# Optimization experiments

Hardware: AMD Instinct MI355X
Metric: run time of the kernel (lower is better)

Reference implementation:

```python
import jax, jax.numpy as jnp
import numpy as np

DIM = 512
NUM_HEADS = 8
HEAD_DIM = DIM // NUM_HEADS
SCALE = HEAD_DIM ** -0.5


def setup_inputs() -> dict:
    key = jax.random.key(0)
    ks = jax.random.split(key, 10)
    B, Sq, Skv = 4, 2048, 2048
    std = DIM ** -0.5
    return {
        "x1": jax.random.normal(ks[0], (B, Sq, DIM), jnp.float32),
        "x2": jax.random.normal(ks[1], (B, Skv, DIM), jnp.float32),
        "Wq": jax.random.normal(ks[2], (DIM, DIM), jnp.float32) * std,
        "bq": jax.random.normal(ks[3], (DIM,), jnp.float32) * 0.02,
        "Wk": jax.random.normal(ks[4], (DIM, DIM), jnp.float32) * std,
        "bk": jax.random.normal(ks[5], (DIM,), jnp.float32) * 0.02,
        "Wv": jax.random.normal(ks[6], (DIM, DIM), jnp.float32) * std,
        "bv": jax.random.normal(ks[7], (DIM,), jnp.float32) * 0.02,
        "Wo": jax.random.normal(ks[8], (DIM, DIM), jnp.float32) * std,
        "bo": jax.random.normal(ks[9], (DIM,), jnp.float32) * 0.02,
    }


def reference(x1, x2, Wq, bq, Wk, bk, Wv, bv, Wo, bo):
    B, Sq, _ = x1.shape
    Skv = x2.shape[1]
    # Linear projections (torch nn.Linear: x @ W.T + b)
    Q = (x1 @ Wq.T + bq).reshape(B, Sq, NUM_HEADS, HEAD_DIM)
    K = (x2 @ Wk.T + bk).reshape(B, Skv, NUM_HEADS, HEAD_DIM)
    V = (x2 @ Wv.T + bv).reshape(B, Skv, NUM_HEADS, HEAD_DIM)
    # [B, H, Sq, Skv]
    attn = jnp.einsum("bqhd,bkhd->bhqk", Q, K) * SCALE
    attn = jax.nn.softmax(attn, axis=-1)  # dropout is identity in eval mode
    out = jnp.einsum("bhqk,bkhd->bqhd", attn, V).reshape(B, Sq, DIM)
    return out @ Wo.T + bo
```

## Files before the change

kernel.cpp:

```cpp
#include <hip/hip_runtime.h>
#include <math.h>

constexpr int kB = 4, kS = 2048, kDim = 512, kNH = 8, kHD = 64;
constexpr float kQScale = 0.18033688011112042f;

using bf16x8 = __attribute__((ext_vector_type(8))) short;
using f32x4  = __attribute__((ext_vector_type(4))) float;

__device__ __forceinline__ unsigned pack_rn(float f0, float f1) {
  unsigned a = __builtin_bit_cast(unsigned, f0) + 0x8000u;
  unsigned b = __builtin_bit_cast(unsigned, f1) + 0x8000u;
  return __builtin_amdgcn_perm(b, a, 0x07060302u);
}
__device__ __forceinline__ unsigned short f2bf_rn(float f) {
  return (unsigned short)((__builtin_bit_cast(unsigned, f) + 0x8000u) >> 16);
}
__device__ __forceinline__ float fexp2(float x) {
#if __has_builtin(__builtin_amdgcn_exp2f)
  return __builtin_amdgcn_exp2f(x);
#else
  return exp2f(x);
#endif
}

#define GLDS(gp, lp) __builtin_amdgcn_global_load_lds(                         \
    (const __attribute__((address_space(1))) void*)(gp),                       \
    (__attribute__((address_space(3))) void*)(lp), 16, 0, 0)

__global__ __launch_bounds__(256) void cvt_bf16(
    const float* __restrict__ x1, const float* __restrict__ x2,
    const float* __restrict__ Wq, const float* __restrict__ Wk,
    const float* __restrict__ Wv, const float* __restrict__ Wo,
    unsigned short* __restrict__ x1b, unsigned short* __restrict__ x2b,
    unsigned short* __restrict__ wb) {
  const size_t i = (size_t)blockIdx.x * 256 + threadIdx.x;
  const float* src;
  unsigned short* dst;
  size_t off;
  if (i < 1048576) { src = x1; dst = x1b; off = i; }
  else if (i < 2097152) { src = x2; dst = x2b; off = i - 1048576; }
  else {
    const size_t j = i - 2097152;
    const int seg = (int)(j >> 16);
    src = seg == 0 ? Wq : seg == 1 ? Wk : seg == 2 ? Wv : Wo;
    dst = wb + (size_t)seg * 262144;
    off = j & 65535;
  }
  const float4 v = *(const float4*)(src + off * 4);
  uint2 o;
  o.x = pack_rn(v.x, v.y);
  o.y = pack_rn(v.z, v.w);
  *(uint2*)(dst + off * 4) = o;
}

__global__ __launch_bounds__(256) void qkv_gemm(
    const unsigned short* __restrict__ x1b, const unsigned short* __restrict__ x2b,
    const unsigned short* __restrict__ wb,
    const float* __restrict__ bq, const float* __restrict__ bk,
    const float* __restrict__ bv,
    unsigned short* __restrict__ Qg, unsigned short* __restrict__ Kg,
    unsigned short* __restrict__ Vg) {
  __shared__ __align__(16) short As0[128 * 32], As1[128 * 32];
  __shared__ __align__(16) short Bs0[128 * 32], Bs1[128 * 32];
  const int z = blockIdx.z;
  const unsigned short* X = z ? x2b : x1b;
  const unsigned short* W = wb + (size_t)z * (kDim * kDim);
  const float* bias = (z == 0) ? bq : (z == 1) ? bk : bv;

  const int t = threadIdx.x, lane = t & 63, w = t >> 6;
  const int g = lane >> 4, c = lane & 15;
  const int bm = blockIdx.y * 128, bn = blockIdx.x * 128;
  const int wm = (w >> 1) * 64, wn = (w & 1) * 64;
  const int lr = lane >> 2, lc = (lane & 3) * 8;

  f32x4 acc[4][4] = {};
  for (int k0 = 0; k0 < kDim; k0 += 64) {
    __syncthreads();
#pragma unroll
    for (int i = 0; i < 2; ++i) {
      const int row = i * 64 + w * 16;
      const size_t ga = (size_t)(bm + row + lr) * kDim + k0 + lc;
      const size_t gb = (size_t)(bn + row + lr) * kDim + k0 + lc;
      GLDS(X + ga, As0 + row * 32);
      GLDS(X + ga + 32, As1 + row * 32);
      GLDS(W + gb, Bs0 + row * 32);
      GLDS(W + gb + 32, Bs1 + row * 32);
    }
    __syncthreads();
#pragma unroll
    for (int kk = 0; kk < 2; ++kk) {
      const short* Ap = kk ? As1 : As0;
      const short* Bp = kk ? Bs1 : Bs0;
      bf16x8 fa[4], fb[4];
      if (z == 2) {
#pragma unroll
        for (int i = 0; i < 4; ++i) fa[i] = *(const bf16x8*)&Ap[(wm + i * 16 + c) * 32 + g * 8];
#pragma unroll
        for (int j = 0; j < 4; ++j) fb[j] = *(const bf16x8*)&Bp[(wn + j * 16 + c) * 32 + g * 8];
      } else {
#pragma unroll
        for (int i = 0; i < 4; ++i) fa[i] = *(const bf16x8*)&Bp[(wn + i * 16 + c) * 32 + g * 8];
#pragma unroll
        for (int j = 0; j < 4; ++j) fb[j] = *(const bf16x8*)&Ap[(wm + j * 16 + c) * 32 + g * 8];
      }
#pragma unroll
      for (int i = 0; i < 4; ++i)
#pragma unroll
        for (int j = 0; j < 4; ++j)
          acc[i][j] = __builtin_amdgcn_mfma_f32_16x16x32_bf16(fa[i], fb[j], acc[i][j], 0, 0, 0);
    }
  }

  if (z == 2) {
#pragma unroll
    for (int tm = 0; tm < 4; ++tm)
#pragma unroll
      for (int tn = 0; tn < 4; ++tn) {
        const int n = bn + wn + tn * 16 + c;
        const float bb = bias[n];
        const int m0 = bm + wm + tm * 16 + g * 4;
        const int b_ = m0 >> 11, s0 = m0 & 2047;
        const int h_ = (n >> 6) & 7, d_ = n & 63;
        uint2 pv;
        pv.x = pack_rn(acc[tm][tn][0] + bb, acc[tm][tn][1] + bb);
        pv.y = pack_rn(acc[tm][tn][2] + bb, acc[tm][tn][3] + bb);
        *(uint2*)(Vg + (((size_t)((b_ * kNH + h_) * kHD + d_)) << 11) + s0) = pv;
      }
  } else {
    const float sc = (z == 0) ? kQScale : 1.0f;
    unsigned short* Og = z ? Kg : Qg;
#pragma unroll
    for (int ti = 0; ti < 4; ++ti) {
      const int n0 = bn + wn + ti * 16 + g * 4;
      const float4 bb = *(const float4*)(bias + n0);
      const int h_ = (n0 >> 6) & 7, d0 = n0 & 63;
#pragma unroll
      for (int tj = 0; tj < 4; ++tj) {
        const int m = bm + wm + tj * 16 + c;
        const int b_ = m >> 11, s_ = m & 2047;
        const f32x4 a = acc[ti][tj];
        uint2 st;
        st.x = pack_rn((a[0] + bb.x) * sc, (a[1] + bb.y) * sc);
        st.y = pack_rn((a[2] + bb.z) * sc, (a[3] + bb.w) * sc);
        *(uint2*)(Og + (((size_t)((b_ * kNH + h_) * kS + s_)) << 6) + d0) = st;
      }
    }
  }
}

__global__ __launch_bounds__(256) void out_gemm(const unsigned short* __restrict__ A,
                                                const unsigned short* __restrict__ Wob,
                                                const float* __restrict__ bias,
                                                float* __restrict__ Y) {
  __shared__ __align__(16) short As0[128 * 32], As1[128 * 32];
  __shared__ __align__(16) short Bs0[64 * 32], Bs1[64 * 32];
  const int t = threadIdx.x, lane = t & 63, w = t >> 6;
  const int g = lane >> 4, c = lane & 15;
  const int bm = blockIdx.y * 128, bn = blockIdx.x * 64;
  const int lr = lane >> 2, lc = (lane & 3) * 8;

  f32x4 acc[4][2] = {};
  for (int k0 = 0; k0 < kDim; k0 += 64) {
    __syncthreads();
#pragma unroll
    for (int i = 0; i < 2; ++i) {
      const int row = i * 64 + w * 16;
      const size_t ga = (size_t)(bm + row + lr) * kDim + k0 + lc;
      GLDS(A + ga, As0 + row * 32);
      GLDS(A + ga + 32, As1 + row * 32);
    }
    {
      const int row = w * 16;
      const size_t gb = (size_t)(bn + row + lr) * kDim + k0 + lc;
      GLDS(Wob + gb, Bs0 + row * 32);
      GLDS(Wob + gb + 32, Bs1 + row * 32);
    }
    __syncthreads();
#pragma unroll
    for (int kk = 0; kk < 2; ++kk) {
      const short* Ap = kk ? As1 : As0;
      const short* Bp = kk ? Bs1 : Bs0;
      bf16x8 fa[4], fb[2];
#pragma unroll
      for (int i = 0; i < 4; ++i) fa[i] = *(const bf16x8*)&Bp[(i * 16 + c) * 32 + g * 8];
#pragma unroll
      for (int j = 0; j < 2; ++j) fb[j] = *(const bf16x8*)&Ap[(w * 32 + j * 16 + c) * 32 + g * 8];
#pragma unroll
      for (int i = 0; i < 4; ++i)
#pragma unroll
        for (int j = 0; j < 2; ++j)
          acc[i][j] = __builtin_amdgcn_mfma_f32_16x16x32_bf16(fa[i], fb[j], acc[i][j], 0, 0, 0);
    }
  }
#pragma unroll
  for (int i = 0; i < 4; ++i) {
    const int n0 = bn + i * 16 + g * 4;
    const float4 bb = *(const float4*)(bias + n0);
#pragma unroll
    for (int j = 0; j < 2; ++j) {
      const int m = bm + w * 32 + j * 16 + c;
      float4 st;
      st.x = acc[i][j][0] + bb.x;
      st.y = acc[i][j][1] + bb.y;
      st.z = acc[i][j][2] + bb.z;
      st.w = acc[i][j][3] + bb.w;
      *(float4*)(Y + (size_t)m * kDim + n0) = st;
    }
  }
}

__global__ __launch_bounds__(256, 4) void flash_mfma(const unsigned short* __restrict__ Qg,
                                                     const unsigned short* __restrict__ Kg,
                                                     const unsigned short* __restrict__ Vg,
                                                     unsigned short* __restrict__ attn) {
  __shared__ __align__(16) short Ks[64 * 76];
  __shared__ __align__(16) short Vs[64 * 76];
  const int t = threadIdx.x, lane = t & 63, w = t >> 6;
  const int c = lane & 15, g4 = lane >> 4;
  const int bh = blockIdx.x, q0 = blockIdx.y * 64;
  const int b_ = bh >> 3, h_ = bh & 7;

  const unsigned short* Qp = Qg + ((size_t)bh * kS + q0) * kHD;
  const unsigned short* Kp = Kg + (size_t)bh * kS * kHD;
  const unsigned short* Vp = Vg + (size_t)bh * kHD * kS;

  bf16x8 bq[2];
  {
    const unsigned short* qr = Qp + (size_t)(w * 16 + c) * kHD + g4 * 8;
    bq[0] = *(const bf16x8*)qr;
    bq[1] = *(const bf16x8*)(qr + 32);
  }

  const int r0 = t >> 3, cc0 = (t & 7) * 8;
  const int ps = (((r0 >> 2) & 1) << 4) | (((r0 >> 3) & 3) << 2) | (r0 & 3);
  const unsigned short* kpt = Kp + (size_t)r0 * kHD + cc0;
  const unsigned short* vpt = Vp + (size_t)r0 * kS + cc0;
  uint4 pk0 = *(const uint4*)kpt;
  uint4 pk1 = *(const uint4*)(kpt + 32 * kHD);
  uint4 pv0 = *(const uint4*)vpt;
  uint4 pv1 = *(const uint4*)(vpt + 32 * kS);
  kpt += 64 * kHD;
  vpt += 64;

  float l = 0.f;
  f32x4 o[4] = {};

  for (int kv0 = 0; kv0 < kS; kv0 += 64) {
    __syncthreads();
    *(uint4*)&Ks[ps * 76 + cc0] = pk0;
    *(uint4*)&Ks[(ps + 32) * 76 + cc0] = pk1;
    *(uint4*)&Vs[r0 * 76 + cc0] = pv0;
    *(uint4*)&Vs[(r0 + 32) * 76 + cc0] = pv1;
    if (kv0 + 64 < kS) {
      pk0 = *(const uint4*)kpt;
      pk1 = *(const uint4*)(kpt + 32 * kHD);
      pv0 = *(const uint4*)vpt;
      pv1 = *(const uint4*)(vpt + 32 * kS);
      kpt += 64 * kHD;
      vpt += 64;
    }
    __syncthreads();

    f32x4 sa[4] = {};
#pragma unroll
    for (int ks = 0; ks < 2; ++ks)
#pragma unroll
      for (int kt = 0; kt < 4; ++kt) {
        const bf16x8 a = *(const bf16x8*)&Ks[(kt * 16 + c) * 76 + ks * 32 + g4 * 8];
        sa[kt] = __builtin_amdgcn_mfma_f32_16x16x32_bf16(a, bq[ks], sa[kt], 0, 0, 0);
      }

#pragma unroll
    for (int ks = 0; ks < 2; ++ks) {
      const float p0 = fexp2(sa[2 * ks][0]), p1 = fexp2(sa[2 * ks][1]);
      const float p2 = fexp2(sa[2 * ks][2]), p3 = fexp2(sa[2 * ks][3]);
      const float p4 = fexp2(sa[2 * ks + 1][0]), p5 = fexp2(sa[2 * ks + 1][1]);
      const float p6 = fexp2(sa[2 * ks + 1][2]), p7 = fexp2(sa[2 * ks + 1][3]);
      l += ((p0 + p1) + (p2 + p3)) + ((p4 + p5) + (p6 + p7));
      uint4 bp;
      bp.x = pack_rn(p0, p1);
      bp.y = pack_rn(p2, p3);
      bp.z = pack_rn(p4, p5);
      bp.w = pack_rn(p6, p7);
      const bf16x8 bpf = __builtin_bit_cast(bf16x8, bp);
#pragma unroll
      for (int dt = 0; dt < 4; ++dt) {
        const bf16x8 va = *(const bf16x8*)&Vs[(dt * 16 + c) * 76 + ks * 32 + g4 * 8];
        o[dt] = __builtin_amdgcn_mfma_f32_16x16x32_bf16(va, bpf, o[dt], 0, 0, 0);
      }
    }
  }

  l += __shfl_xor(l, 16, 64);
  l += __shfl_xor(l, 32, 64);
  const float inv = 1.0f / l;
  unsigned short* orow = attn + ((size_t)(b_ * kS + q0 + w * 16 + c)) * kDim + h_ * kHD;
#pragma unroll
  for (int dt = 0; dt < 4; ++dt) {
    uint2 st;
    st.x = pack_rn(o[dt][0] * inv, o[dt][1] * inv);
    st.y = pack_rn(o[dt][2] * inv, o[dt][3] * inv);
    *(uint2*)(orow + dt * 16 + g4 * 4) = st;
  }
}

extern "C" void kernel_launch(void* const* d_in, const int* in_sizes, int n_in,
                              void* d_out, int out_size, void* d_ws, size_t ws_size,
                              hipStream_t stream) {
  const float* x1 = (const float*)d_in[0];
  const float* x2 = (const float*)d_in[1];
  const float* Wq = (const float*)d_in[2];
  const float* bq = (const float*)d_in[3];
  const float* Wk = (const float*)d_in[4];
  const float* bk = (const float*)d_in[5];
  const float* Wv = (const float*)d_in[6];
  const float* bv = (const float*)d_in[7];
  const float* Wo = (const float*)d_in[8];
  const float* bo = (const float*)d_in[9];
  float* out = (float*)d_out;

  constexpr size_t kTok = (size_t)kB * kS * kDim;
  unsigned short* x1b = (unsigned short*)d_ws;
  unsigned short* x2b = x1b + kTok;
  unsigned short* wb  = x2b + kTok;
  unsigned short* Qg  = wb + 4 * (size_t)(kDim * kDim);
  unsigned short* Kg  = Qg + kTok;
  unsigned short* Vg  = Kg + kTok;
  unsigned short* atb = Vg + kTok;

  const dim3 blk(256);
  cvt_bf16<<<dim3(9216), blk, 0, stream>>>(x1, x2, Wq, Wk, Wv, Wo, x1b, x2b, wb);
  qkv_gemm<<<dim3(4, 64, 3), blk, 0, stream>>>(x1b, x2b, wb, bq, bk, bv, Qg, Kg, Vg);
  flash_mfma<<<dim3(32, 32), blk, 0, stream>>>(Qg, Kg, Vg, atb);
  out_gemm<<<dim3(8, 64), blk, 0, stream>>>(atb, wb + 3 * (size_t)(kDim * kDim), bo, out);
}
```

Measured before the change: 193.6 us.

## Use 32x32 MFMA with split-KV waves in attention; shrink GEMM tiles

The attention kernel moves from 16x16x32 to 32x32x16 MFMA. Each wave now covers 32 queries over half of each 64-key tile, and the two halves' partial outputs and row sums are combined through shared memory at the end. The K-tile swizzle is changed to match the new access pattern. Separately, the QKV GEMM tile is narrowed to 128x64 and the output GEMM tile to 64x64, which doubles the grid sizes for more parallelism but lowers per-block data reuse. The attention change adds a final reduction and barrier, and relies on the new swizzle avoiding LDS bank conflicts.

```diff
diff --git a/kernel.cpp b/kernel.cpp
--- a/kernel.cpp
+++ b/kernel.cpp
@@ -6,14 +6,12 @@
 
 using bf16x8 = __attribute__((ext_vector_type(8))) short;
 using f32x4  = __attribute__((ext_vector_type(4))) float;
+using f32x16 = __attribute__((ext_vector_type(16))) float;
 
 __device__ __forceinline__ unsigned pack_rn(float f0, float f1) {
   unsigned a = __builtin_bit_cast(unsigned, f0) + 0x8000u;
   unsigned b = __builtin_bit_cast(unsigned, f1) + 0x8000u;
   return __builtin_amdgcn_perm(b, a, 0x07060302u);
-}
-__device__ __forceinline__ unsigned short f2bf_rn(float f) {
-  return (unsigned short)((__builtin_bit_cast(unsigned, f) + 0x8000u) >> 16);
 }
 __device__ __forceinline__ float fexp2(float x) {
 #if __has_builtin(__builtin_amdgcn_exp2f)
@@ -61,7 +59,7 @@
     unsigned short* __restrict__ Qg, unsigned short* __restrict__ Kg,
     unsigned short* __restrict__ Vg) {
   __shared__ __align__(16) short As0[128 * 32], As1[128 * 32];
-  __shared__ __align__(16) short Bs0[128 * 32], Bs1[128 * 32];
+  __shared__ __align__(16) short Bs0[64 * 32], Bs1[64 * 32];
   const int z = blockIdx.z;
   const unsigned short* X = z ? x2b : x1b;
   const unsigned short* W = wb + (size_t)z * (kDim * kDim);
@@ -69,20 +67,22 @@
 
   const int t = threadIdx.x, lane = t & 63, w = t >> 6;
   const int g = lane >> 4, c = lane & 15;
-  const int bm = blockIdx.y * 128, bn = blockIdx.x * 128;
-  const int wm = (w >> 1) * 64, wn = (w & 1) * 64;
+  const int bm = blockIdx.y * 128, bn = blockIdx.x * 64;
   const int lr = lane >> 2, lc = (lane & 3) * 8;
 
-  f32x4 acc[4][4] = {};
+  f32x4 acc[8] = {};
   for (int k0 = 0; k0 < kDim; k0 += 64) {
     __syncthreads();
 #pragma unroll
     for (int i = 0; i < 2; ++i) {
       const int row = i * 64 + w * 16;
       const size_t ga = (size_t)(bm + row + lr) * kDim + k0 + lc;
-      const size_t gb = (size_t)(bn + row + lr) * kDim + k0 + lc;
       GLDS(X + ga, As0 + row * 32);
       GLDS(X + ga + 32, As1 + row * 32);
+    }
+    {
+      const int row = w * 16;
+      const size_t gb = (size_t)(bn + row + lr) * kDim + k0 + lc;
       GLDS(W + gb, Bs0 + row * 32);
       GLDS(W + gb + 32, Bs1 + row * 32);
     }
@@ -91,54 +91,65 @@
     for (int kk = 0; kk < 2; ++kk) {
       const short* Ap = kk ? As1 : As0;
       const short* Bp = kk ? Bs1 : Bs0;
-      bf16x8 fa[4], fb[4];
       if (z == 2) {
-#pragma unroll
-        for (int i = 0; i < 4; ++i) fa[i] = *(const bf16x8*)&Ap[(wm + i * 16 + c) * 32 + g * 8];
-#pragma unroll
-        for (int j = 0; j < 4; ++j) fb[j] = *(const bf16x8*)&Bp[(wn + j * 16 + c) * 32 + g * 8];
+        bf16x8 fa[2], fb[4];
+#pragma unroll
+        for (int i = 0; i < 2; ++i) fa[i] = *(const bf16x8*)&Ap[(w * 32 + i * 16 + c) * 32 + g * 8];
+#pragma unroll
+        for (int j = 0; j < 4; ++j) fb[j] = *(const bf16x8*)&Bp[(j * 16 + c) * 32 + g * 8];
+#pragma unroll
+        for (int i = 0; i < 2; ++i)
+#pragma unroll
+          for (int j = 0; j < 4; ++j)
+            acc[i * 4 + j] = __builtin_amdgcn_mfma_f32_16x16x32_bf16(fa[i], fb[j], acc[i * 4 + j], 0, 0, 0);
       } else {
-#pragma unroll
-        for (int i = 0; i < 4; ++i) fa[i] = *(const bf16x8*)&Bp[(wn + i * 16 + c) * 32 + g * 8];
-#pragma unroll
-        for (int j = 0; j < 4; ++j) fb[j] = *(const bf16x8*)&Ap[(wm + j * 16 + c) * 32 + g * 8];
+        bf16x8 fa[4], fb[2];
+#pragma unroll
+        for (int i = 0; i < 4; ++i) fa[i] = *(const bf16x8*)&Bp[(i * 16 + c) * 32 + g * 8];
+#pragma unroll
+        for (int j = 0; j < 2; ++j) fb[j] = *(const bf16x8*)&Ap[(w * 32 + j * 16 + c) * 32 + g * 8];
+#pragma unroll
+        for (int i = 0; i < 4; ++i)
+#pragma unroll
+          for (int j = 0; j < 2; ++j)
+            acc[i * 2 + j] = __builtin_amdgcn_mfma_f32_16x16x32_bf16(fa[i], fb[j], acc[i * 2 + j], 0, 0, 0);
       }
-#pragma unroll
-      for (int i = 0; i < 4; ++i)
-#pragma unroll
-        for (int j = 0; j < 4; ++j)
-          acc[i][j] = __builtin_amdgcn_mfma_f32_16x16x32_bf16(fa[i], fb[j], acc[i][j], 0, 0, 0);
-    }
-  }
-
+    }
+  }
+
+  const int bh_base = 0;
+  (void)bh_base;
   if (z == 2) {
-#pragma unroll
-    for (int tm = 0; tm < 4; ++tm)
-#pragma unroll
-      for (int tn = 0; tn < 4; ++tn) {
-        const int n = bn + wn + tn * 16 + c;
+    const int h_ = bn >> 6;
+#pragma unroll
+    for (int i = 0; i < 2; ++i)
+#pragma unroll
+      for (int j = 0; j < 4; ++j) {
+        const int n = bn + j * 16 + c;
         const float bb = bias[n];
-        const int m0 = bm + wm + tm * 16 + g * 4;
+        const int m0 = bm + w * 32 + i * 16 + g * 4;
         const int b_ = m0 >> 11, s0 = m0 & 2047;
-        const int h_ = (n >> 6) & 7, d_ = n & 63;
+        const int d_ = n & 63;
+        const f32x4 a = acc[i * 4 + j];
         uint2 pv;
-        pv.x = pack_rn(acc[tm][tn][0] + bb, acc[tm][tn][1] + bb);
-        pv.y = pack_rn(acc[tm][tn][2] + bb, acc[tm][tn][3] + bb);
+        pv.x = pack_rn(a[0] + bb, a[1] + bb);
+        pv.y = pack_rn(a[2] + bb, a[3] + bb);
         *(uint2*)(Vg + (((size_t)((b_ * kNH + h_) * kHD + d_)) << 11) + s0) = pv;
       }
   } else {
     const float sc = (z == 0) ? kQScale : 1.0f;
     unsigned short* Og = z ? Kg : Qg;
-#pragma unroll
-    for (int ti = 0; ti < 4; ++ti) {
-      const int n0 = bn + wn + ti * 16 + g * 4;
+    const int h_ = bn >> 6;
+#pragma unroll
+    for (int i = 0; i < 4; ++i) {
+      const int n0 = bn + i * 16 + g * 4;
       const float4 bb = *(const float4*)(bias + n0);
-      const int h_ = (n0 >> 6) & 7, d0 = n0 & 63;
-#pragma unroll
-      for (int tj = 0; tj < 4; ++tj) {
-        const int m = bm + wm + tj * 16 + c;
+      const int d0 = n0 & 63;
+#pragma unroll
+      for (int j = 0; j < 2; ++j) {
+        const int m = bm + w * 32 + j * 16 + c;
         const int b_ = m >> 11, s_ = m & 2047;
-        const f32x4 a = acc[ti][tj];
+        const f32x4 a = acc[i * 2 + j];
         uint2 st;
         st.x = pack_rn((a[0] + bb.x) * sc, (a[1] + bb.y) * sc);
         st.y = pack_rn((a[2] + bb.z) * sc, (a[3] + bb.w) * sc);
@@ -152,26 +163,23 @@
                                                 const unsigned short* __restrict__ Wob,
                                                 const float* __restrict__ bias,
                                                 float* __restrict__ Y) {
-  __shared__ __align__(16) short As0[128 * 32], As1[128 * 32];
+  __shared__ __align__(16) short As0[64 * 32], As1[64 * 32];
   __shared__ __align__(16) short Bs0[64 * 32], Bs1[64 * 32];
   const int t = threadIdx.x, lane = t & 63, w = t >> 6;
   const int g = lane >> 4, c = lane & 15;
-  const int bm = blockIdx.y * 128, bn = blockIdx.x * 64;
+  const int bm = blockIdx.y * 64, bn = blockIdx.x * 64;
+  const int wm = (w >> 1) * 32, wn = (w & 1) * 32;
   const int lr = lane >> 2, lc = (lane & 3) * 8;
 
-  f32x4 acc[4][2] = {};
+  f32x4 acc[2][2] = {};
   for (int k0 = 0; k0 < kDim; k0 += 64) {
     __syncthreads();
-#pragma unroll
-    for (int i = 0; i < 2; ++i) {
-      const int row = i * 64 + w * 16;
+    {
+      const int row = w * 16;
       const size_t ga = (size_t)(bm + row + lr) * kDim + k0 + lc;
+      const size_t gb = (size_t)(bn + row + lr) * kDim + k0 + lc;
       GLDS(A + ga, As0 + row * 32);
       GLDS(A + ga + 32, As1 + row * 32);
-    }
-    {
-      const int row = w * 16;
-      const size_t gb = (size_t)(bn + row + lr) * kDim + k0 + lc;
       GLDS(Wob + gb, Bs0 + row * 32);
       GLDS(Wob + gb + 32, Bs1 + row * 32);
     }
@@ -180,25 +188,25 @@
     for (int kk = 0; kk < 2; ++kk) {
       const short* Ap = kk ? As1 : As0;
       const short* Bp = kk ? Bs1 : Bs0;
-      bf16x8 fa[4], fb[2];
-#pragma unroll
-      for (int i = 0; i < 4; ++i) fa[i] = *(const bf16x8*)&Bp[(i * 16 + c) * 32 + g * 8];
-#pragma unroll
-      for (int j = 0; j < 2; ++j) fb[j] = *(const bf16x8*)&Ap[(w * 32 + j * 16 + c) * 32 + g * 8];
-#pragma unroll
-      for (int i = 0; i < 4; ++i)
+      bf16x8 fa[2], fb[2];
+#pragma unroll
+      for (int i = 0; i < 2; ++i) fa[i] = *(const bf16x8*)&Bp[(wn + i * 16 + c) * 32 + g * 8];
+#pragma unroll
+      for (int j = 0; j < 2; ++j) fb[j] = *(const bf16x8*)&Ap[(wm + j * 16 + c) * 32 + g * 8];
+#pragma unroll
+      for (int i = 0; i < 2; ++i)
 #pragma unroll
         for (int j = 0; j < 2; ++j)
           acc[i][j] = __builtin_amdgcn_mfma_f32_16x16x32_bf16(fa[i], fb[j], acc[i][j], 0, 0, 0);
     }
   }
 #pragma unroll
-  for (int i = 0; i < 4; ++i) {
-    const int n0 = bn + i * 16 + g * 4;
+  for (int i = 0; i < 2; ++i) {
+    const int n0 = bn + wn + i * 16 + g * 4;
     const float4 bb = *(const float4*)(bias + n0);
 #pragma unroll
     for (int j = 0; j < 2; ++j) {
-      const int m = bm + w * 32 + j * 16 + c;
+      const int m = bm + wm + j * 16 + c;
       float4 st;
       st.x = acc[i][j][0] + bb.x;
       st.y = acc[i][j][1] + bb.y;
@@ -213,10 +221,12 @@
                                                      const unsigned short* __restrict__ Kg,
                                                      const unsigned short* __restrict__ Vg,
                                                      unsigned short* __restrict__ attn) {
-  __shared__ __align__(16) short Ks[64 * 76];
-  __shared__ __align__(16) short Vs[64 * 76];
+  __shared__ __align__(16) short SMEM[2 * 64 * 76];
+  short* const Ks = SMEM;
+  short* const Vs = SMEM + 64 * 76;
   const int t = threadIdx.x, lane = t & 63, w = t >> 6;
-  const int c = lane & 15, g4 = lane >> 4;
+  const int c32 = lane & 31, g2 = lane >> 5;
+  const int qh = w & 1, kh = w >> 1;
   const int bh = blockIdx.x, q0 = blockIdx.y * 64;
   const int b_ = bh >> 3, h_ = bh & 7;
 
@@ -224,15 +234,15 @@
   const unsigned short* Kp = Kg + (size_t)bh * kS * kHD;
   const unsigned short* Vp = Vg + (size_t)bh * kHD * kS;
 
-  bf16x8 bq[2];
+  bf16x8 bq[4];
   {
-    const unsigned short* qr = Qp + (size_t)(w * 16 + c) * kHD + g4 * 8;
-    bq[0] = *(const bf16x8*)qr;
-    bq[1] = *(const bf16x8*)(qr + 32);
+    const unsigned short* qr = Qp + (size_t)(qh * 32 + c32) * kHD + g2 * 8;
+#pragma unroll
+    for (int ks = 0; ks < 4; ++ks) bq[ks] = *(const bf16x8*)(qr + ks * 16);
   }
 
   const int r0 = t >> 3, cc0 = (t & 7) * 8;
-  const int ps = (((r0 >> 2) & 1) << 4) | (((r0 >> 3) & 3) << 2) | (r0 & 3);
+  const int ps = r0 ^ ((((r0 >> 2) ^ (r0 >> 3)) & 1) * 12);
   const unsigned short* kpt = Kp + (size_t)r0 * kHD + cc0;
   const unsigned short* vpt = Vp + (size_t)r0 * kS + cc0;
   uint4 pk0 = *(const uint4*)kpt;
@@ -243,7 +253,7 @@
   vpt += 64;
 
   float l = 0.f;
-  f32x4 o[4] = {};
+  f32x16 o0 = {}, o1 = {};
 
   for (int kv0 = 0; kv0 < kS; kv0 += 64) {
     __syncthreads();
@@ -261,21 +271,19 @@
     }
     __syncthreads();
 
-    f32x4 sa[4] = {};
-#pragma unroll
-    for (int ks = 0; ks < 2; ++ks)
-#pragma unroll
-      for (int kt = 0; kt < 4; ++kt) {
-        const bf16x8 a = *(const bf16x8*)&Ks[(kt * 16 + c) * 76 + ks * 32 + g4 * 8];
-        sa[kt] = __builtin_amdgcn_mfma_f32_16x16x32_bf16(a, bq[ks], sa[kt], 0, 0, 0);
-      }
-
-#pragma unroll
-    for (int ks = 0; ks < 2; ++ks) {
-      const float p0 = fexp2(sa[2 * ks][0]), p1 = fexp2(sa[2 * ks][1]);
-      const float p2 = fexp2(sa[2 * ks][2]), p3 = fexp2(sa[2 * ks][3]);
-      const float p4 = fexp2(sa[2 * ks + 1][0]), p5 = fexp2(sa[2 * ks + 1][1]);
-      const float p6 = fexp2(sa[2 * ks + 1][2]), p7 = fexp2(sa[2 * ks + 1][3]);
+    f32x16 sa = {};
+#pragma unroll
+    for (int ks = 0; ks < 4; ++ks) {
+      const bf16x8 a = *(const bf16x8*)&Ks[(kh * 32 + c32) * 76 + ks * 16 + g2 * 8];
+      sa = __builtin_amdgcn_mfma_f32_32x32x16_bf16(a, bq[ks], sa, 0, 0, 0);
+    }
+
+#pragma unroll
+    for (int kp = 0; kp < 2; ++kp) {
+      const float p0 = fexp2(sa[kp * 8 + 0]), p1 = fexp2(sa[kp * 8 + 1]);
+      const float p2 = fexp2(sa[kp * 8 + 2]), p3 = fexp2(sa[kp * 8 + 3]);
+      const float p4 = fexp2(sa[kp * 8 + 4]), p5 = fexp2(sa[kp * 8 + 5]);
+      const float p6 = fexp2(sa[kp * 8 + 6]), p7 = fexp2(sa[kp * 8 + 7]);
       l += ((p0 + p1) + (p2 + p3)) + ((p4 + p5) + (p6 + p7));
       uint4 bp;
       bp.x = pack_rn(p0, p1);
@@ -283,24 +291,48 @@
       bp.z = pack_rn(p4, p5);
       bp.w = pack_rn(p6, p7);
       const bf16x8 bpf = __builtin_bit_cast(bf16x8, bp);
-#pragma unroll
-      for (int dt = 0; dt < 4; ++dt) {
-        const bf16x8 va = *(const bf16x8*)&Vs[(dt * 16 + c) * 76 + ks * 32 + g4 * 8];
-        o[dt] = __builtin_amdgcn_mfma_f32_16x16x32_bf16(va, bpf, o[dt], 0, 0, 0);
+      const bf16x8 va0 = *(const bf16x8*)&Vs[c32 * 76 + kh * 32 + kp * 16 + g2 * 8];
+      const bf16x8 va1 = *(const bf16x8*)&Vs[(32 + c32) * 76 + kh * 32 + kp * 16 + g2 * 8];
+      o0 = __builtin_amdgcn_mfma_f32_32x32x16_bf16(va0, bpf, o0, 0, 0, 0);
+      o1 = __builtin_amdgcn_mfma_f32_32x32x16_bf16(va1, bpf, o1, 0, 0, 0);
+    }
+  }
+
+  l += __shfl_xor(l, 32, 64);
+  __syncthreads();
+  float2* oscr = (float2*)SMEM;
+  float* lscr = (float*)SMEM + 4096;
+  if (kh == 1) {
+#pragma unroll
+    for (int r2 = 0; r2 < 8; ++r2) {
+      oscr[qh * 1024 + r2 * 64 + lane]       = make_float2(o0[2 * r2], o0[2 * r2 + 1]);
+      oscr[qh * 1024 + 512 + r2 * 64 + lane] = make_float2(o1[2 * r2], o1[2 * r2 + 1]);
+    }
+    lscr[qh * 64 + lane] = l;
+  }
+  __syncthreads();
+  if (kh == 0) {
+#pragma unroll
+    for (int r2 = 0; r2 < 8; ++r2) {
+      const float2 a = oscr[qh * 1024 + r2 * 64 + lane];
+      const float2 b = oscr[qh * 1024 + 512 + r2 * 64 + lane];
+      o0[2 * r2] += a.x; o0[2 * r2 + 1] += a.y;
+      o1[2 * r2] += b.x; o1[2 * r2 + 1] += b.y;
+    }
+    l += lscr[qh * 64 + lane];
+    const float inv = 1.0f / l;
+    unsigned short* orow = attn + ((size_t)(b_ * kS + q0 + qh * 32 + c32)) * kDim + h_ * kHD;
+#pragma unroll
+    for (int dt = 0; dt < 2; ++dt) {
+      const f32x16 oo = dt ? o1 : o0;
+#pragma unroll
+      for (int rg = 0; rg < 4; ++rg) {
+        uint2 st;
+        st.x = pack_rn(oo[rg * 4 + 0] * inv, oo[rg * 4 + 1] * inv);
+        st.y = pack_rn(oo[rg * 4 + 2] * inv, oo[rg * 4 + 3] * inv);
+        *(uint2*)(orow + dt * 32 + 8 * rg + 4 * g2) = st;
       }
     }
-  }
-
-  l += __shfl_xor(l, 16, 64);
-  l += __shfl_xor(l, 32, 64);
-  const float inv = 1.0f / l;
-  unsigned short* orow = attn + ((size_t)(b_ * kS + q0 + w * 16 + c)) * kDim + h_ * kHD;
-#pragma unroll
-  for (int dt = 0; dt < 4; ++dt) {
-    uint2 st;
-    st.x = pack_rn(o[dt][0] * inv, o[dt][1] * inv);
-    st.y = pack_rn(o[dt][2] * inv, o[dt][3] * inv);
-    *(uint2*)(orow + dt * 16 + g4 * 4) = st;
   }
 }
 
@@ -330,7 +362,7 @@
 
   const dim3 blk(256);
   cvt_bf16<<<dim3(9216), blk, 0, stream>>>(x1, x2, Wq, Wk, Wv, Wo, x1b, x2b, wb);
-  qkv_gemm<<<dim3(4, 64, 3), blk, 0, stream>>>(x1b, x2b, wb, bq, bk, bv, Qg, Kg, Vg);
+  qkv_gemm<<<dim3(8, 64, 3), blk, 0, stream>>>(x1b, x2b, wb, bq, bk, bv, Qg, Kg, Vg);
   flash_mfma<<<dim3(32, 32), blk, 0, stream>>>(Qg, Kg, Vg, atb);
-  out_gemm<<<dim3(8, 64), blk, 0, stream>>>(atb, wb + 3 * (size_t)(kDim * kDim), bo, out);
-}
+  out_gemm<<<dim3(8, 128), blk, 0, stream>>>(atb, wb + 3 * (size_t)(kDim * kDim), bo, out);
+}
```

Result: slower. 293.1 us (+51.4%).
